# Optimization experiments

Measured on AMD Instinct MI355X. Metric: run time of the kernel, lower is better.

The kernel has to match this reference:

```python
import jax, jax.numpy as jnp
import numpy as np
from functools import partial

G, N, E = 512, 256, 1024
F_IN, EMB, H, NCLS = 30, 256, 3, 2
NEG_SLOPE = 0.2
K1 = int(np.ceil(0.8 * N))   # 205
K2 = int(np.ceil(0.8 * K1))  # 164
K3 = int(np.ceil(0.8 * K2))  # 132


def _gat(x, src, dst, emask, W, asrc, adst, b):
    # Single-graph GATConv (PyG semantics, eval mode): x [n,f], edges [e] + validity mask.
    # Adds self-loops (PyG default), edge-softmax grouped by destination node.
    n = x.shape[0]
    h = (x @ W.T).reshape(n, H, EMB)                      # [n,H,C]
    a_s = (h * asrc).sum(-1)                              # [n,H]
    a_d = (h * adst).sum(-1)                              # [n,H]
    loops = jnp.arange(n, dtype=src.dtype)
    s = jnp.concatenate([src, loops])
    d = jnp.concatenate([dst, loops])
    m = jnp.concatenate([emask, jnp.ones((n,), bool)])
    logit = jax.nn.leaky_relu(a_s[s] + a_d[d], NEG_SLOPE)  # [e+n,H]
    logit = jnp.where(m[:, None], logit, -1e9)
    mx = jax.ops.segment_max(logit, d, num_segments=n)     # stable softmax per dst
    w = jnp.exp(logit - mx[d]) * m[:, None]
    den = jax.ops.segment_sum(w, d, num_segments=n)
    alpha = w / den[d]
    out = jax.ops.segment_sum(alpha[:, :, None] * h[s], d, num_segments=n)  # [n,H,C]
    return out.reshape(n, H * EMB) + b


def _pool(x, src, dst, emask, p, k):
    # TopKPooling: score = tanh((x.p)/||p||); keep top-k nodes, scale by score,
    # remap edge indices and invalidate edges touching dropped nodes.
    n = x.shape[0]
    score = jnp.tanh((x @ p) / jnp.linalg.norm(p))
    vals, perm = jax.lax.top_k(score, k)
    xn = x[perm] * vals[:, None]
    inv = jnp.full((n,), -1, jnp.int32).at[perm].set(jnp.arange(k, dtype=jnp.int32))
    ns, nd = inv[src], inv[dst]
    nm = emask & (ns >= 0) & (nd >= 0)
    return xn, jnp.maximum(ns, 0), jnp.maximum(nd, 0), nm


_gat_b = jax.vmap(_gat, in_axes=(0, 0, 0, 0, None, None, None, None))


def _pool_b(x, src, dst, m, p, k):
    return jax.vmap(partial(_pool, k=k), in_axes=(0, 0, 0, 0, None))(x, src, dst, m, p)


def _readout(x):
    # global_max_pool || global_mean_pool per graph: [G,n,d] -> [G,2d]
    return jnp.concatenate([x.max(axis=1), x.mean(axis=1)], axis=-1)


def _forward(x, edge_src, edge_dst, params):
    (W1, as1, ad1, b1, ht1w, ht1b, p1,
     W2, as2, ad2, b2, ht2w, ht2b, p2,
     W3, as3, ad3, b3, ht3w, ht3b, p3,
     l1w, l1b, l2w, l2b) = params
    src, dst = edge_src, edge_dst
    m = jnp.ones(src.shape, bool)
    h = _gat_b(x, src, dst, m, W1, as1, ad1, b1) @ ht1w.T + ht1b
    h, src, dst, m = _pool_b(h, src, dst, m, p1, K1)
    x1 = _readout(h)
    h = _gat_b(h, src, dst, m, W2, as2, ad2, b2) @ ht2w.T + ht2b
    h, src, dst, m = _pool_b(h, src, dst, m, p2, K2)
    x2 = _readout(h)
    h = _gat_b(h, src, dst, m, W3, as3, ad3, b3) @ ht3w.T + ht3b
    h, src, dst, m = _pool_b(h, src, dst, m, p3, K3)
    x3 = _readout(h)
    z = x1 + x2 + x3
    z = jax.nn.relu(z @ l1w.T + l1b)  # F.dropout is a no-op in eval mode
    return z @ l2w.T + l2b


def setup_inputs() -> dict:
    key = jax.random.key(0)
    keys = iter(jax.random.split(key, 64))
    def nrm(shape, s=0.05):
        return jax.random.normal(next(keys), shape, jnp.float32) * s
    inp = {
        "x": jax.random.normal(next(keys), (G, N, F_IN), jnp.float32),
        "edge_src": jax.random.randint(next(keys), (G, E), 0, N, jnp.int32),
        "edge_dst": jax.random.randint(next(keys), (G, E), 0, N, jnp.int32),
    }
    for i, fin in ((1, F_IN), (2, EMB), (3, EMB)):
        inp[f"W{i}"] = nrm((H * EMB, fin))
        inp[f"asrc{i}"] = nrm((H, EMB))
        inp[f"adst{i}"] = nrm((H, EMB))
        inp[f"b{i}"] = jnp.zeros((H * EMB,), jnp.float32)
        inp[f"ht{i}_w"] = nrm((EMB, H * EMB))
        inp[f"ht{i}_b"] = jnp.zeros((EMB,), jnp.float32)
        inp[f"p{i}"] = nrm((EMB,), 1.0)
    inp["lin1_w"] = nrm((EMB, 2 * EMB))
    inp["lin1_b"] = jnp.zeros((EMB,), jnp.float32)
    inp["lin2_w"] = nrm((NCLS, EMB))
    inp["lin2_b"] = jnp.zeros((NCLS,), jnp.float32)
    return inp


def reference(x, edge_src, edge_dst,
              W1, asrc1, adst1, b1, ht1_w, ht1_b, p1,
              W2, asrc2, adst2, b2, ht2_w, ht2_b, p2,
              W3, asrc3, adst3, b3, ht3_w, ht3_b, p3,
              lin1_w, lin1_b, lin2_w, lin2_b):
    params = (W1, asrc1, adst1, b1, ht1_w, ht1_b, p1,
              W2, asrc2, adst2, b2, ht2_w, ht2_b, p2,
              W3, asrc3, adst3, b3, ht3_w, ht3_b, p3,
              lin1_w, lin1_b, lin2_w, lin2_b)
    return _forward(x, edge_src, edge_dst, params)
```

## Files before the change

kernel.cpp:

```cpp
#include <hip/hip_runtime.h>
#include <hip/hip_bf16.h>

#define GG 512
#define NMAX 256
#define EE 1024
#define HH 3
#define EMB 256
#define NEDGE 1280
#define NEG 0.2f

typedef __attribute__((ext_vector_type(8))) short bf16x8;
typedef __attribute__((ext_vector_type(4))) float f32x4;
#define MFMA16(A,B,C) __builtin_amdgcn_mfma_f32_16x16x32_bf16((A),(B),(C),0,0,0)

__device__ inline void bsplit(float v, unsigned short& s0, unsigned short& s1,
                              unsigned short& s2) {
  __hip_bfloat16 b0 = __float2bfloat16(v);
  float r1 = v - __bfloat162float(b0);
  __hip_bfloat16 b1 = __float2bfloat16(r1);
  float r2 = r1 - __bfloat162float(b1);
  __hip_bfloat16 b2 = __float2bfloat16(r2);
  s0 = *(unsigned short*)&b0; s1 = *(unsigned short*)&b1; s2 = *(unsigned short*)&b2;
}

__global__ void k_prep_wa(const float* __restrict__ W, const float* __restrict__ asrc,
                          const float* __restrict__ adst, float* __restrict__ wa_s,
                          float* __restrict__ wa_d, int f) {
  int t = blockIdx.x * blockDim.x + threadIdx.x;
  int tot = HH * f;
  if (t >= 2 * tot) return;
  int which = t / tot;
  int r = t - which * tot;
  int hd = r / f, ff = r - hd * f;
  const float* a = which ? adst : asrc;
  float s = 0.f;
  for (int c = 0; c < EMB; ++c)
    s += a[hd * EMB + c] * W[(size_t)(hd * EMB + c) * f + ff];
  (which ? wa_d : wa_s)[r] = s;
}

__global__ void k_prep_mcatP(const float* __restrict__ W, const float* __restrict__ htw,
                             float* __restrict__ mcat, int f, int KP) {
  int t = blockIdx.x * blockDim.x + threadIdx.x;
  if (t >= KP * EMB) return;
  int row = t >> 8, j = t & 255;
  float s = 0.f;
  if (row < 3 * f) {
    int hd = row / f, ff = row - hd * f;
    for (int c = 0; c < EMB; ++c)
      s += htw[(size_t)j * (HH * EMB) + hd * EMB + c] * W[(size_t)(hd * EMB + c) * f + ff];
  }
  mcat[(size_t)row * EMB + j] = s;
}

__global__ void k_prep_bt3(const float* __restrict__ mcat, unsigned short* __restrict__ B0,
                           unsigned short* __restrict__ B1, unsigned short* __restrict__ B2,
                           int KP) {
  int t = blockIdx.x * blockDim.x + threadIdx.x;
  if (t >= 256 * KP) return;
  int n = t / KP, k = t - n * KP;
  float v = mcat[(size_t)k * 256 + n];
  unsigned short s0, s1, s2;
  bsplit(v, s0, s1, s2);
  B0[t] = s0; B1[t] = s1; B2[t] = s2;
}

__global__ void k_prep_bb(const float* __restrict__ b, const float* __restrict__ htw,
                          const float* __restrict__ htb, float* __restrict__ bb) {
  int j = threadIdx.x;
  float s = htb[j];
  for (int k = 0; k < HH * EMB; ++k) s += b[k] * htw[(size_t)j * (HH * EMB) + k];
  bb[j] = s;
}

__global__ void k_prep_q(const float* __restrict__ mcat, const float* __restrict__ p,
                         double* __restrict__ qv, int f) {
  int r = blockIdx.x * blockDim.x + threadIdx.x;
  if (r >= 3 * f) return;
  double s = 0.0;
  for (int c = 0; c < EMB; ++c) s += (double)mcat[(size_t)r * EMB + c] * (double)p[c];
  qv[r] = s;
}

__global__ void k_prep_sc(const float* __restrict__ p, const float* __restrict__ bb,
                          double* __restrict__ sc2) {
  __shared__ double sh[256], sh2[256];
  int t = threadIdx.x;
  double pv = (double)p[t];
  sh[t] = pv * pv;
  sh2[t] = (double)bb[t] * pv;
  __syncthreads();
  for (int s = 128; s > 0; s >>= 1) {
    if (t < s) { sh[t] += sh[t + s]; sh2[t] += sh2[t + s]; }
    __syncthreads();
  }
  if (t == 0) { sc2[0] = sh2[0]; sc2[1] = sqrt(sh[0]); }
}

__global__ __launch_bounds__(256) void k_graph(
    const int* __restrict__ src_in, const int* __restrict__ dst_in, int first,
    int* __restrict__ es, int* __restrict__ ed, int* __restrict__ em,
    const float* __restrict__ xin, const float* __restrict__ wa_s,
    const float* __restrict__ wa_d, const double* __restrict__ qv,
    const double* __restrict__ sc2,
    float4* __restrict__ a4, int* __restrict__ coff, int* __restrict__ elist,
    int* __restrict__ sel, float* __restrict__ val, int n_in, int f, int kout) {
  __shared__ float lgs[NEDGE * 3];
  __shared__ unsigned short sdst[NEDGE], ssrc[NEDGE];
  __shared__ unsigned char sval[NEDGE];
  __shared__ float sas[256][3], sad[256][3];
  __shared__ double stdt[256][3];
  __shared__ int cnt2[256];
  __shared__ int scn[256];
  __shared__ int off[257];
  __shared__ int elist_s[NEDGE];
  __shared__ float sscore[256];
  __shared__ unsigned long long keys[256];
  __shared__ int inv[256];
  int g = blockIdx.x, tid = threadIdx.x;
  int etot = EE + n_in;
  cnt2[tid] = 0;
  if (tid < n_in) {
    const float* xr = xin + ((size_t)g * n_in + tid) * f;
    float s0 = 0, s1 = 0, s2 = 0, d0 = 0, d1 = 0, d2 = 0;
    double t0 = 0, t1 = 0, t2 = 0;
    for (int c = 0; c < f; ++c) {
      float xv = xr[c];
      s0 += xv * wa_s[c]; s1 += xv * wa_s[f + c]; s2 += xv * wa_s[2 * f + c];
      d0 += xv * wa_d[c]; d1 += xv * wa_d[f + c]; d2 += xv * wa_d[2 * f + c];
      double xd = (double)xv;
      t0 += xd * qv[c]; t1 += xd * qv[f + c]; t2 += xd * qv[2 * f + c];
    }
    sas[tid][0] = s0; sas[tid][1] = s1; sas[tid][2] = s2;
    sad[tid][0] = d0; sad[tid][1] = d1; sad[tid][2] = d2;
    stdt[tid][0] = t0; stdt[tid][1] = t1; stdt[tid][2] = t2;
  }
  __syncthreads();
  for (int e = tid; e < etot; e += 256) {
    int s, d, v;
    if (e < EE) {
      if (first) { s = src_in[g * EE + e]; d = dst_in[g * EE + e]; v = 1; }
      else { s = es[g * EE + e]; d = ed[g * EE + e]; v = em[g * EE + e]; }
    } else { s = d = e - EE; v = 1; }
    sdst[e] = (unsigned short)d; ssrc[e] = (unsigned short)s; sval[e] = (unsigned char)v;
    if (v) {
#pragma unroll
      for (int h = 0; h < HH; ++h) {
        float lv = sas[s][h] + sad[d][h];
        lgs[e * 3 + h] = lv > 0.f ? lv : NEG * lv;
      }
      atomicAdd(&cnt2[d], 1);
    }
  }
  __syncthreads();
  scn[tid] = cnt2[tid];
  __syncthreads();
  for (int d = 1; d < 256; d <<= 1) {
    int t = (tid >= d) ? scn[tid - d] : 0;
    __syncthreads();
    scn[tid] += t;
    __syncthreads();
  }
  off[tid + 1] = scn[tid];
  if (tid == 0) off[0] = 0;
  __syncthreads();
  for (int i = tid; i <= n_in; i += 256) coff[g * 257 + i] = off[i];
  cnt2[tid] = 0;
  __syncthreads();
  for (int e = tid; e < etot; e += 256) {
    if (sval[e]) {
      int d = sdst[e];
      int pos = atomicAdd(&cnt2[d], 1);
      elist_s[off[d] + pos] = e;
    }
  }
  __syncthreads();
  if (tid < n_in) {
    int o0 = off[tid], o1 = off[tid + 1];
    for (int i = o0 + 1; i < o1; ++i) {
      int key = elist_s[i];
      int j = i - 1;
      while (j >= o0 && elist_s[j] > key) { elist_s[j + 1] = elist_s[j]; --j; }
      elist_s[j + 1] = key;
    }
    for (int q = o0; q < o1; ++q) elist[g * NEDGE + q] = elist_s[q];
  }
  __syncthreads();
  float sc = -3e38f;
  if (tid < n_in) {
    int o0 = off[tid], o1 = off[tid + 1];
    float m0 = -1e30f, m1 = -1e30f, m2 = -1e30f;
    for (int q = o0; q < o1; ++q) {
      int e = elist_s[q];
      m0 = fmaxf(m0, lgs[e * 3 + 0]);
      m1 = fmaxf(m1, lgs[e * 3 + 1]);
      m2 = fmaxf(m2, lgs[e * 3 + 2]);
    }
    float d0 = 0, d1 = 0, d2 = 0;
    for (int q = o0; q < o1; ++q) {
      int e = elist_s[q];
      d0 += expf(lgs[e * 3 + 0] - m0);
      d1 += expf(lgs[e * 3 + 1] - m1);
      d2 += expf(lgs[e * 3 + 2] - m2);
    }
    float r0 = 1.f / d0, r1 = 1.f / d1, r2 = 1.f / d2;
    double s = 0.0;
    for (int q = o0; q < o1; ++q) {
      int e = elist_s[q];
      float w0 = expf(lgs[e * 3 + 0] - m0) * r0;
      float w1 = expf(lgs[e * 3 + 1] - m1) * r1;
      float w2 = expf(lgs[e * 3 + 2] - m2) * r2;
      int src = ssrc[e];
      float4 av; av.x = w0; av.y = w1; av.z = w2; av.w = __int_as_float(src);
      a4[(size_t)g * NEDGE + e] = av;
      s += (double)w0 * stdt[src][0] + (double)w1 * stdt[src][1] + (double)w2 * stdt[src][2];
    }
    sc = (float)tanh((s + sc2[0]) / sc2[1]);
  }
  sscore[tid] = sc;
  unsigned int u = __float_as_uint(sc);
  unsigned int ord = (u & 0x80000000u) ? ~u : (u | 0x80000000u);
  unsigned long long key = ((unsigned long long)(~ord) << 32) | (unsigned int)tid;
  if (tid >= n_in) key = 0xFFFFFFFF00000000ull | (unsigned int)tid;
  keys[tid] = key;
  __syncthreads();
  for (int kk = 2; kk <= 256; kk <<= 1) {
    for (int j = kk >> 1; j > 0; j >>= 1) {
      int ixj = tid ^ j;
      if (ixj > tid) {
        unsigned long long a = keys[tid], b = keys[ixj];
        bool up = ((tid & kk) == 0);
        if (up ? (a > b) : (a < b)) { keys[tid] = b; keys[ixj] = a; }
      }
      __syncthreads();
    }
  }
  inv[tid] = -1;
  __syncthreads();
  if (tid < kout) {
    int pi = (int)(keys[tid] & 0xFFFFu);
    inv[pi] = tid;
    sel[g * 256 + tid] = pi;
    val[g * 256 + tid] = sscore[pi];
  }
  __syncthreads();
  for (int e = tid; e < EE; e += 256) {
    int s = ssrc[e], d = sdst[e], m = sval[e];
    int ns = inv[s], nd = inv[d];
    int nm = (m && ns >= 0 && nd >= 0) ? 1 : 0;
    es[g * EE + e] = ns < 0 ? 0 : ns;
    ed[g * EE + e] = nd < 0 ? 0 : nd;
    em[g * EE + e] = nm;
  }
}

template<bool F256>
__global__ __launch_bounds__(256) void k_gather_sel(
    const float* __restrict__ xin, const float4* __restrict__ a4,
    const int* __restrict__ coff, const int* __restrict__ elist,
    const int* __restrict__ sel,
    unsigned short* __restrict__ A0, unsigned short* __restrict__ A1,
    unsigned short* __restrict__ A2,
    int gc, int n_in, int n_out, int f, int KP) {
  int wid = (blockIdx.x * blockDim.x + threadIdx.x) >> 6;
  int lane = threadIdx.x & 63;
  if (wid >= gc * n_out) return;
  int g = wid / n_out, j = wid - g * n_out;
  int pi = sel[(g << 8) + j];
  int o0 = coff[g * 257 + pi], o1 = coff[g * 257 + pi + 1];
  const float* xg = xin + (size_t)g * n_in * f;
  size_t rb = ((size_t)g * n_out + j) * (size_t)KP;
  if (F256) {
    float4 acc0 = make_float4(0, 0, 0, 0);
    float4 acc1 = make_float4(0, 0, 0, 0);
    float4 acc2 = make_float4(0, 0, 0, 0);
    for (int t = o0; t < o1; ++t) {
      int e = elist[g * NEDGE + t];
      float4 a = a4[(size_t)g * NEDGE + e];
      int src = __float_as_int(a.w);
      float4 xv = ((const float4*)(xg + (size_t)src * 256))[lane];
      acc0.x += a.x * xv.x; acc0.y += a.x * xv.y; acc0.z += a.x * xv.z; acc0.w += a.x * xv.w;
      acc1.x += a.y * xv.x; acc1.y += a.y * xv.y; acc1.z += a.y * xv.z; acc1.w += a.y * xv.w;
      acc2.x += a.z * xv.x; acc2.y += a.z * xv.y; acc2.z += a.z * xv.z; acc2.w += a.z * xv.w;
    }
    float4 accs[3] = {acc0, acc1, acc2};
#pragma unroll
    for (int h = 0; h < 3; ++h) {
      size_t idx = rb + (size_t)h * 256 + lane * 4;
      ushort4 u0, u1, u2;
      bsplit(accs[h].x, u0.x, u1.x, u2.x);
      bsplit(accs[h].y, u0.y, u1.y, u2.y);
      bsplit(accs[h].z, u0.z, u1.z, u2.z);
      bsplit(accs[h].w, u0.w, u1.w, u2.w);
      *(ushort4*)&A0[idx] = u0;
      *(ushort4*)&A1[idx] = u1;
      *(ushort4*)&A2[idx] = u2;
    }
  } else {
    for (int kk = lane; kk < 96; kk += 64) {
      float v = 0.f;
      if (kk < 90) {
        int h = kk / 30, cc = kk - h * 30;
        for (int t = o0; t < o1; ++t) {
          int e = elist[g * NEDGE + t];
          float4 a = a4[(size_t)g * NEDGE + e];
          int src = __float_as_int(a.w);
          float al = (h == 0) ? a.x : ((h == 1) ? a.y : a.z);
          v += al * xg[(size_t)src * 30 + cc];
        }
      }
      unsigned short s0, s1, s2;
      bsplit(v, s0, s1, s2);
      A0[rb + kk] = s0; A1[rb + kk] = s1; A2[rb + kk] = s2;
    }
  }
}

__global__ __launch_bounds__(256) void k_mgemm(
    const unsigned short* __restrict__ A0, const unsigned short* __restrict__ A1,
    const unsigned short* __restrict__ A2,
    const unsigned short* __restrict__ B0, const unsigned short* __restrict__ B1,
    const unsigned short* __restrict__ B2,
    const float* __restrict__ bias, const float* __restrict__ val,
    float* __restrict__ xout, int Mrows, int KP, int n_out, int nbx) {
  __shared__ unsigned short As[3][64 * 32];
  __shared__ unsigned short Bs[3][64 * 32];
  int tid = threadIdx.x;
  int jj = blockIdx.x & 31;
  int rr0 = (blockIdx.x >> 5) * 8 + (jj & 7);
  int cc0 = jj >> 3;
  if (rr0 >= nbx) return;
  int row0 = rr0 * 64;
  int col0 = cc0 * 64;
  int lane = tid & 63, w = tid >> 6;
  int kg = lane >> 4, r16 = lane & 15;
  int wr = (w >> 1) * 32, wc = (w & 1) * 32;
  int sr = tid >> 2, sj = tid & 3;
  int sp = sj ^ ((sr >> 1) & 3);
  const unsigned short* Ap[3] = {A0, A1, A2};
  const unsigned short* Bp[3] = {B0, B1, B2};

  f32x4 acc[2][2];
#pragma unroll
  for (int i = 0; i < 2; ++i)
#pragma unroll
    for (int j = 0; j < 2; ++j) acc[i][j] = (f32x4){0.f, 0.f, 0.f, 0.f};

  int nkt = KP >> 5;
  for (int kt = 0; kt < nkt; ++kt) {
    int k0 = kt << 5;
    int gra = row0 + sr;
    int grb = col0 + sr;
#pragma unroll
    for (int p = 0; p < 3; ++p) {
      uint4 va = make_uint4(0, 0, 0, 0);
      if (gra < Mrows) va = *(const uint4*)&Ap[p][(size_t)gra * KP + k0 + (sj << 3)];
      *(uint4*)&As[p][sr * 32 + (sp << 3)] = va;
      uint4 vb = *(const uint4*)&Bp[p][(size_t)grb * KP + k0 + (sj << 3)];
      *(uint4*)&Bs[p][sr * 32 + (sp << 3)] = vb;
    }
    __syncthreads();
    bf16x8 af[2][3], bf[2][3];
#pragma unroll
    for (int fm = 0; fm < 2; ++fm) {
      int row = wr + (fm << 4) + r16;
      int pk = kg ^ ((row >> 1) & 3);
#pragma unroll
      for (int p = 0; p < 3; ++p)
        af[fm][p] = *(const bf16x8*)&As[p][row * 32 + (pk << 3)];
    }
#pragma unroll
    for (int fn = 0; fn < 2; ++fn) {
      int col = wc + (fn << 4) + r16;
      int pk = kg ^ ((col >> 1) & 3);
#pragma unroll
      for (int p = 0; p < 3; ++p)
        bf[fn][p] = *(const bf16x8*)&Bs[p][col * 32 + (pk << 3)];
    }
#pragma unroll
    for (int fm = 0; fm < 2; ++fm)
#pragma unroll
      for (int fn = 0; fn < 2; ++fn) {
        f32x4 c = acc[fm][fn];
        c = MFMA16(af[fm][0], bf[fn][0], c);
        c = MFMA16(af[fm][0], bf[fn][1], c);
        c = MFMA16(af[fm][1], bf[fn][0], c);
        c = MFMA16(af[fm][0], bf[fn][2], c);
        c = MFMA16(af[fm][2], bf[fn][0], c);
        c = MFMA16(af[fm][1], bf[fn][1], c);
        acc[fm][fn] = c;
      }
    __syncthreads();
  }
#pragma unroll
  for (int fm = 0; fm < 2; ++fm)
#pragma unroll
    for (int fn = 0; fn < 2; ++fn) {
      int colg = col0 + wc + (fn << 4) + r16;
      float bi = bias[colg];
#pragma unroll
      for (int rr = 0; rr < 4; ++rr) {
        int rowg = row0 + wr + (fm << 4) + (kg << 2) + rr;
        if (rowg < Mrows) {
          int gg = rowg / n_out, j = rowg - gg * n_out;
          xout[((size_t)gg * n_out + j) * EMB + colg] =
              (acc[fm][fn][rr] + bi) * val[(gg << 8) + j];
        }
      }
    }
}

__global__ void k_readout(const float* __restrict__ x, float* __restrict__ z,
                          int n_out, int g0) {
  int g = blockIdx.x, c = threadIdx.x;
  float mx = -3e38f, sm = 0.f;
  for (int j = 0; j < n_out; ++j) {
    float v = x[((size_t)g * n_out + j) * EMB + c];
    mx = fmaxf(mx, v);
    sm += v;
  }
  z[(size_t)(g0 + g) * 512 + c] += mx;
  z[(size_t)(g0 + g) * 512 + 256 + c] += sm / (float)n_out;
}

__global__ void k_mlp(const float* __restrict__ z, const float* __restrict__ l1w,
                      const float* __restrict__ l1b, const float* __restrict__ l2w,
                      const float* __restrict__ l2b, float* __restrict__ out) {
  __shared__ float zs[512];
  __shared__ float h1[256];
  int g = blockIdx.x, tid = threadIdx.x;
  zs[tid] = z[(size_t)g * 512 + tid];
  zs[256 + tid] = z[(size_t)g * 512 + 256 + tid];
  __syncthreads();
  float s = l1b[tid];
  for (int c = 0; c < 512; ++c) s += zs[c] * l1w[(size_t)tid * 512 + c];
  h1[tid] = s > 0.f ? s : 0.f;
  __syncthreads();
  if (tid < 2) {
    float o = l2b[tid];
    for (int c = 0; c < 256; ++c) o += h1[c] * l2w[(size_t)tid * 256 + c];
    out[g * 2 + tid] = o;
  }
}

extern "C" void kernel_launch(void* const* d_in, const int* in_sizes, int n_in_cnt,
                              void* d_out, int out_size, void* d_ws, size_t ws_size,
                              hipStream_t stream) {
  (void)in_sizes; (void)n_in_cnt; (void)out_size;
  const float* x0 = (const float*)d_in[0];
  const int* e_src = (const int*)d_in[1];
  const int* e_dst = (const int*)d_in[2];
  struct LP { const float *W, *as, *ad, *b, *hw, *hb, *p; int f, nin, nout, KP; };
  LP L[3];
  for (int l = 0; l < 3; ++l) {
    int base = 3 + l * 7;
    L[l].W  = (const float*)d_in[base + 0];
    L[l].as = (const float*)d_in[base + 1];
    L[l].ad = (const float*)d_in[base + 2];
    L[l].b  = (const float*)d_in[base + 3];
    L[l].hw = (const float*)d_in[base + 4];
    L[l].hb = (const float*)d_in[base + 5];
    L[l].p  = (const float*)d_in[base + 6];
  }
  L[0].f = 30;  L[1].f = 256; L[2].f = 256;
  L[0].nin = 256; L[0].nout = 205; L[0].KP = 96;
  L[1].nin = 205; L[1].nout = 164; L[1].KP = 768;
  L[2].nin = 164; L[2].nout = 132; L[2].KP = 768;
  const float* l1w = (const float*)d_in[24];
  const float* l1b = (const float*)d_in[25];
  const float* l2w = (const float*)d_in[26];
  const float* l2b = (const float*)d_in[27];
  float* out = (float*)d_out;

  char* w = (char*)d_ws;
  char* wend = w + ws_size;
  auto alloc = [&](size_t bytes) {
    char* r = w; w += (bytes + 255) & ~(size_t)255; return r;
  };
  float*  z = (float*)alloc((size_t)GG * 512 * 4);
  float *wa_s[3], *wa_d[3], *mcatP[3], *bbv[3];
  unsigned short *bt0[3], *bt1[3], *bt2[3];
  double *qv[3], *sc2[3];
  for (int l = 0; l < 3; ++l) {
    int KP = (l == 0) ? 96 : 768;
    wa_s[l]  = (float*)alloc((size_t)HH * 256 * 4);
    wa_d[l]  = (float*)alloc((size_t)HH * 256 * 4);
    mcatP[l] = (float*)alloc((size_t)768 * EMB * 4);
    bbv[l]   = (float*)alloc((size_t)EMB * 4);
    bt0[l]   = (unsigned short*)alloc((size_t)256 * KP * 2);
    bt1[l]   = (unsigned short*)alloc((size_t)256 * KP * 2);
    bt2[l]   = (unsigned short*)alloc((size_t)256 * KP * 2);
    qv[l]    = (double*)alloc((size_t)768 * 8);
    sc2[l]   = (double*)alloc(256);
  }

  const size_t AMAX = (size_t)164 * 768;
  const size_t APAD = (size_t)64 * 768;
  size_t fixed_used = (size_t)(w - (char*)d_ws);
  size_t per_g = (size_t)205 * EMB * 4
               + AMAX * 2 * 3
               + (size_t)NEDGE * 16
               + (size_t)EE * 4 * 3
               + (size_t)257 * 4 + (size_t)NEDGE * 4
               + (size_t)256 * 4 * 2
               + 24 * 256;
  size_t avail = (ws_size > fixed_used + 1048576) ? (ws_size - fixed_used - 1048576) : 0;
  int Gc = (int)(avail / per_g);
  if (Gc > GG) Gc = GG;
  if (Gc < 1) Gc = 1;
  int nchunks = (GG + Gc - 1) / Gc;
  Gc = (GG + nchunks - 1) / nchunks;

  float*  xbuf = (float*)alloc((size_t)Gc * 205 * EMB * 4);
  unsigned short* AP0 = (unsigned short*)alloc(((size_t)Gc * AMAX + APAD) * 2);
  unsigned short* AP1 = (unsigned short*)alloc(((size_t)Gc * AMAX + APAD) * 2);
  unsigned short* AP2 = (unsigned short*)alloc(((size_t)Gc * AMAX + APAD) * 2);
  float4* a4   = (float4*)alloc((size_t)Gc * NEDGE * 16);
  int*    es   = (int*)alloc((size_t)Gc * EE * 4);
  int*    ed   = (int*)alloc((size_t)Gc * EE * 4);
  int*    em   = (int*)alloc((size_t)Gc * EE * 4);
  int*    coff = (int*)alloc((size_t)Gc * 257 * 4);
  int*    elist= (int*)alloc((size_t)Gc * NEDGE * 4);
  int*    sel  = (int*)alloc((size_t)Gc * 256 * 4);
  float*  val  = (float*)alloc((size_t)Gc * 256 * 4);
  if (w > wend) return;

  (void)hipMemsetAsync(z, 0, (size_t)GG * 512 * 4, stream);

  for (int l = 0; l < 3; ++l) {
    int f = L[l].f, KP = L[l].KP;
    k_prep_wa<<<(2 * HH * f + 255) / 256, 256, 0, stream>>>(L[l].W, L[l].as, L[l].ad, wa_s[l], wa_d[l], f);
    k_prep_mcatP<<<(KP * EMB + 255) / 256, 256, 0, stream>>>(L[l].W, L[l].hw, mcatP[l], f, KP);
    k_prep_bt3<<<(256 * KP + 255) / 256, 256, 0, stream>>>(mcatP[l], bt0[l], bt1[l], bt2[l], KP);
    k_prep_bb<<<1, 256, 0, stream>>>(L[l].b, L[l].hw, L[l].hb, bbv[l]);
    k_prep_q<<<(3 * f + 255) / 256, 256, 0, stream>>>(mcatP[l], L[l].p, qv[l], f);
    k_prep_sc<<<1, 256, 0, stream>>>(L[l].p, bbv[l], sc2[l]);
  }

  for (int g0 = 0; g0 < GG; g0 += Gc) {
    int gc = (GG - g0 < Gc) ? (GG - g0) : Gc;
    const float* xin = x0 + (size_t)g0 * 256 * 30;
    for (int l = 0; l < 3; ++l) {
      int f = L[l].f, nin = L[l].nin, nout = L[l].nout, KP = L[l].KP;
      k_graph<<<gc, 256, 0, stream>>>(e_src + (size_t)g0 * EE, e_dst + (size_t)g0 * EE,
                                      (l == 0) ? 1 : 0, es, ed, em,
                                      xin, wa_s[l], wa_d[l], qv[l], sc2[l],
                                      a4, coff, elist, sel, val, nin, f, nout);
      { int waves = gc * nout;
        if (f == 256)
          k_gather_sel<true><<<(waves * 64 + 255) / 256, 256, 0, stream>>>(
              xin, a4, coff, elist, sel, AP0, AP1, AP2, gc, nin, nout, f, KP);
        else
          k_gather_sel<false><<<(waves * 64 + 255) / 256, 256, 0, stream>>>(
              xin, a4, coff, elist, sel, AP0, AP1, AP2, gc, nin, nout, f, KP);
      }
      { int Mrows = gc * nout;
        int nbx = (Mrows + 63) / 64;
        int nblk = ((nbx + 7) / 8) * 32;
        k_mgemm<<<nblk, 256, 0, stream>>>(AP0, AP1, AP2, bt0[l], bt1[l], bt2[l],
                                          bbv[l], val, xbuf, Mrows, KP, nout, nbx);
      }
      k_readout<<<gc, 256, 0, stream>>>(xbuf, z, nout, g0);
      xin = xbuf;
    }
  }
  k_mlp<<<GG, 256, 0, stream>>>(z, l1w, l1b, l2w, l2b, out);
}
```

Before: 1.829 ms.

## Store GEMM operands in fragment-tiled layout and load MFMA fragments directly from global

The gather and weight-prep kernels now write the split-bf16 A and B operands in a 16-row by 8-k tiled layout that matches the MFMA fragment shape. The GEMM kernel drops its shared-memory staging and both barriers, and loads each fragment straight from global memory as one contiguous 16-byte vector per lane. This removes LDS traffic and synchronisation, but every wave now reads its operands from global or L2 with no sharing inside the block. The M-row bounds check on A loads is also gone, which relies on padded buffers.

```diff
diff --git a/kernel.cpp b/kernel.cpp
--- a/kernel.cpp
+++ b/kernel.cpp
@@ -12,6 +12,10 @@
 typedef __attribute__((ext_vector_type(8))) short bf16x8;
 typedef __attribute__((ext_vector_type(4))) float f32x4;
 #define MFMA16(A,B,C) __builtin_amdgcn_mfma_f32_16x16x32_bf16((A),(B),(C),0,0,0)
+
+__device__ __forceinline__ size_t ftidx(int row, int k, int kp8) {
+  return (((size_t)(row >> 4) * kp8 + (k >> 3)) << 7) + ((row & 15) << 3) + (k & 7);
+}
 
 __device__ inline void bsplit(float v, unsigned short& s0, unsigned short& s1,
                               unsigned short& s2) {
@@ -62,7 +66,8 @@
   float v = mcat[(size_t)k * 256 + n];
   unsigned short s0, s1, s2;
   bsplit(v, s0, s1, s2);
-  B0[t] = s0; B1[t] = s1; B2[t] = s2;
+  size_t idx = ftidx(n, k, KP >> 3);
+  B0[idx] = s0; B1[idx] = s1; B2[idx] = s2;
 }
 
 __global__ void k_prep_bb(const float* __restrict__ b, const float* __restrict__ htw,
@@ -269,7 +274,8 @@
   int pi = sel[(g << 8) + j];
   int o0 = coff[g * 257 + pi], o1 = coff[g * 257 + pi + 1];
   const float* xg = xin + (size_t)g * n_in * f;
-  size_t rb = ((size_t)g * n_out + j) * (size_t)KP;
+  int grow = g * n_out + j;
+  int kp8 = KP >> 3;
   if (F256) {
     float4 acc0 = make_float4(0, 0, 0, 0);
     float4 acc1 = make_float4(0, 0, 0, 0);
@@ -286,7 +292,8 @@
     float4 accs[3] = {acc0, acc1, acc2};
 #pragma unroll
     for (int h = 0; h < 3; ++h) {
-      size_t idx = rb + (size_t)h * 256 + lane * 4;
+      int k0 = h * 256 + lane * 4;
+      size_t idx = ftidx(grow, k0, kp8);
       ushort4 u0, u1, u2;
       bsplit(accs[h].x, u0.x, u1.x, u2.x);
       bsplit(accs[h].y, u0.y, u1.y, u2.y);
@@ -311,7 +318,8 @@
       }
       unsigned short s0, s1, s2;
       bsplit(v, s0, s1, s2);
-      A0[rb + kk] = s0; A1[rb + kk] = s1; A2[rb + kk] = s2;
+      size_t idx = ftidx(grow, kk, kp8);
+      A0[idx] = s0; A1[idx] = s1; A2[idx] = s2;
     }
   }
 }
@@ -323,8 +331,6 @@
     const unsigned short* __restrict__ B2,
     const float* __restrict__ bias, const float* __restrict__ val,
     float* __restrict__ xout, int Mrows, int KP, int n_out, int nbx) {
-  __shared__ unsigned short As[3][64 * 32];
-  __shared__ unsigned short Bs[3][64 * 32];
   int tid = threadIdx.x;
   int jj = blockIdx.x & 31;
   int rr0 = (blockIdx.x >> 5) * 8 + (jj & 7);
@@ -335,8 +341,9 @@
   int lane = tid & 63, w = tid >> 6;
   int kg = lane >> 4, r16 = lane & 15;
   int wr = (w >> 1) * 32, wc = (w & 1) * 32;
-  int sr = tid >> 2, sj = tid & 3;
-  int sp = sj ^ ((sr >> 1) & 3);
+  int kp8 = KP >> 3;
+  int arb0 = (row0 + wr) >> 4;
+  int brb0 = (col0 + wc) >> 4;
   const unsigned short* Ap[3] = {A0, A1, A2};
   const unsigned short* Bp[3] = {B0, B1, B2};
 
@@ -348,34 +355,21 @@
 
   int nkt = KP >> 5;
   for (int kt = 0; kt < nkt; ++kt) {
-    int k0 = kt << 5;
-    int gra = row0 + sr;
-    int grb = col0 + sr;
-#pragma unroll
-    for (int p = 0; p < 3; ++p) {
-      uint4 va = make_uint4(0, 0, 0, 0);
-      if (gra < Mrows) va = *(const uint4*)&Ap[p][(size_t)gra * KP + k0 + (sj << 3)];
-      *(uint4*)&As[p][sr * 32 + (sp << 3)] = va;
-      uint4 vb = *(const uint4*)&Bp[p][(size_t)grb * KP + k0 + (sj << 3)];
-      *(uint4*)&Bs[p][sr * 32 + (sp << 3)] = vb;
-    }
-    __syncthreads();
+    int kb = (kt << 2) + kg;
     bf16x8 af[2][3], bf[2][3];
 #pragma unroll
     for (int fm = 0; fm < 2; ++fm) {
-      int row = wr + (fm << 4) + r16;
-      int pk = kg ^ ((row >> 1) & 3);
+      size_t base = (((size_t)(arb0 + fm) * kp8 + kb) << 7) + (r16 << 3);
 #pragma unroll
       for (int p = 0; p < 3; ++p)
-        af[fm][p] = *(const bf16x8*)&As[p][row * 32 + (pk << 3)];
+        af[fm][p] = *(const bf16x8*)&Ap[p][base];
     }
 #pragma unroll
     for (int fn = 0; fn < 2; ++fn) {
-      int col = wc + (fn << 4) + r16;
-      int pk = kg ^ ((col >> 1) & 3);
+      size_t base = (((size_t)(brb0 + fn) * kp8 + kb) << 7) + (r16 << 3);
 #pragma unroll
       for (int p = 0; p < 3; ++p)
-        bf[fn][p] = *(const bf16x8*)&Bs[p][col * 32 + (pk << 3)];
+        bf[fn][p] = *(const bf16x8*)&Bp[p][base];
     }
 #pragma unroll
     for (int fm = 0; fm < 2; ++fm)
@@ -390,7 +384,6 @@
         c = MFMA16(af[fm][1], bf[fn][1], c);
         acc[fm][fn] = c;
       }
-    __syncthreads();
   }
 #pragma unroll
   for (int fm = 0; fm < 2; ++fm)
```

New measurement: 2.125 ms. 1.16x slower.
